# Kernel optimization log

Measured on AMD Instinct MI355X. Metric: run time of the kernel, lower is better.

The kernel has to match this reference:

```python
import jax, jax.numpy as jnp
import numpy as np

N_NODES = 50000
N_EDGES = 600000
N_GRAPHS = 500
HID = 128
N_LAYERS = 3
N_CLASSES = 10


def setup_inputs() -> dict:
    key = jax.random.key(0)
    ks = jax.random.split(key, 10)
    x = jax.random.normal(ks[0], (N_NODES, HID), dtype=jnp.float32)
    edge_attr = jax.random.normal(ks[1], (N_EDGES, 4), dtype=jnp.float32)
    edge_index = jax.random.randint(ks[2], (2, N_EDGES), 0, N_NODES, dtype=jnp.int32)
    batch = jnp.sort(jax.random.randint(ks[3], (N_NODES,), 0, N_GRAPHS, dtype=jnp.int32))
    s = 1.0 / np.sqrt(HID)
    Wl = jax.random.normal(ks[4], (N_LAYERS, HID, HID), dtype=jnp.float32) * s
    bl = jax.random.normal(ks[5], (N_LAYERS, HID), dtype=jnp.float32) * s
    Wr = jax.random.normal(ks[6], (N_LAYERS, HID, HID), dtype=jnp.float32) * s
    W1 = jax.random.normal(ks[7], (HID, HID), dtype=jnp.float32) * s
    b1 = jnp.zeros((HID,), dtype=jnp.float32)
    W2 = jax.random.normal(ks[8], (N_CLASSES, HID), dtype=jnp.float32) * s
    b2 = jnp.zeros((N_CLASSES,), dtype=jnp.float32)
    return {"x": x, "edge_attr": edge_attr, "edge_index": edge_index, "batch": batch,
            "Wl": Wl, "bl": bl, "Wr": Wr, "W1": W1, "b1": b1, "W2": W2, "b2": b2}


def _sage_conv(x, src, dst, Wl_i, bl_i, Wr_i):
    # mean aggregation of source-node features at target nodes (PyG SAGEConv)
    msg_sum = jax.ops.segment_sum(x[src], dst, num_segments=N_NODES)  # [N, H]
    cnt = jax.ops.segment_sum(jnp.ones((src.shape[0],), x.dtype), dst, num_segments=N_NODES)
    mean = msg_sum / jnp.maximum(cnt, 1.0)[:, None]
    return mean @ Wl_i.T + bl_i + x @ Wr_i.T


def reference(x, edge_attr, edge_index, batch, Wl, bl, Wr, W1, b1, W2, b2):
    # edge_attr is ignored by SAGEConv
    src, dst = edge_index[0], edge_index[1]
    for i in range(N_LAYERS):
        x = jax.nn.relu(_sage_conv(x, src, dst, Wl[i], bl[i], Wr[i]))
    # global_add_pool over graphs
    g = jax.ops.segment_sum(x, batch, num_segments=N_GRAPHS)  # [G, H]
    g = jax.nn.relu(g)
    # dropout p=0.5 is identity at inference
    h = jax.nn.relu(g @ W1.T + b1)
    logits = h @ W2.T + b2
    return jax.nn.log_softmax(logits, axis=1)
```

## Files before the change

### kernel.cpp

```cpp
#include <hip/hip_runtime.h>
#include <math.h>

#define HID 128
#define NCLS 10
#define MAXDEG 32
#define TROWS 64
#define MSP 136

typedef __attribute__((ext_vector_type(8))) short frag8;
typedef __attribute__((ext_vector_type(8))) unsigned short u16x8;
typedef __attribute__((ext_vector_type(2))) unsigned int u32x2;
typedef __attribute__((ext_vector_type(4))) float f32x4;

static __device__ __forceinline__ float relu_f(float v) { return v > 0.f ? v : 0.f; }

static __device__ __forceinline__ unsigned short f2bf(float f) {
    unsigned int u = __float_as_uint(f);
    u += 0x7fffu + ((u >> 16) & 1u);
    return (unsigned short)(u >> 16);
}
static __device__ __forceinline__ float bf2f(unsigned short u) {
    return __uint_as_float(((unsigned int)u) << 16);
}

static __device__ __forceinline__ unsigned int f2fp8x4(float a, float b, float c, float d) {
    int w = __builtin_amdgcn_cvt_pk_fp8_f32(a, b, 0, false);
    w = __builtin_amdgcn_cvt_pk_fp8_f32(c, d, w, true);
    return (unsigned int)w;
}
static __device__ __forceinline__ unsigned char f2fp8(float v) {
    return (unsigned char)(__builtin_amdgcn_cvt_pk_fp8_f32(v, v, 0, false) & 0xff);
}
static __device__ __forceinline__ void f8acc(unsigned int w0, unsigned int w1, float* acc) {
    auto p0 = __builtin_amdgcn_cvt_pk_f32_fp8((int)w0, false);
    auto p1 = __builtin_amdgcn_cvt_pk_f32_fp8((int)w0, true);
    auto p2 = __builtin_amdgcn_cvt_pk_f32_fp8((int)w1, false);
    auto p3 = __builtin_amdgcn_cvt_pk_f32_fp8((int)w1, true);
    acc[0] += p0[0]; acc[1] += p0[1]; acc[2] += p1[0]; acc[3] += p1[1];
    acc[4] += p2[0]; acc[5] += p2[1]; acc[6] += p3[0]; acc[7] += p3[1];
}

static __device__ __forceinline__ void conv4(const float* __restrict__ in,
                                             unsigned short* __restrict__ out, int i) {
    float4 v = *(const float4*)&in[i * 4];
    ushort4 o;
    o.x = f2bf(v.x); o.y = f2bf(v.y); o.z = f2bf(v.z); o.w = f2bf(v.w);
    *(ushort4*)&out[i * 4] = o;
}

__global__ __launch_bounds__(256) void prep_kernel(const float* __restrict__ x, unsigned short* __restrict__ xb,
                                                   unsigned int* __restrict__ xf8w, int nx4,
                                                   const float* __restrict__ Wl, unsigned short* __restrict__ wlb, int nwl4,
                                                   const float* __restrict__ Wr, unsigned short* __restrict__ wrb, int nwr4,
                                                   int* __restrict__ deg, int ndeg4,
                                                   uint4* __restrict__ colp, int ncol8, unsigned int zpat,
                                                   uint4* __restrict__ zp0, uint4* __restrict__ zp1,
                                                   uint4* __restrict__ zp2, int nz8,
                                                   uint4* __restrict__ zf0, uint4* __restrict__ zf1,
                                                   uint4* __restrict__ zf2) {
    int i = blockIdx.x * blockDim.x + threadIdx.x;
    if (i < nx4) {
        float4 v = *(const float4*)&x[i * 4];
        ushort4 o;
        o.x = f2bf(v.x); o.y = f2bf(v.y); o.z = f2bf(v.z); o.w = f2bf(v.w);
        *(ushort4*)&xb[i * 4] = o;
        xf8w[i] = f2fp8x4(v.x, v.y, v.z, v.w);
        return;
    }
    i -= nx4;
    if (i < nwl4) { conv4(Wl, wlb, i); return; }
    i -= nwl4;
    if (i < nwr4) { conv4(Wr, wrb, i); return; }
    i -= nwr4;
    if (i < ndeg4) { *(int4*)&deg[i * 4] = make_int4(0, 0, 0, 0); return; }
    i -= ndeg4;
    if (i < ncol8) { colp[i] = make_uint4(zpat, zpat, zpat, zpat); return; }
    i -= ncol8;
    if (i < nz8) { zp0[i] = make_uint4(0, 0, 0, 0); return; }
    i -= nz8;
    if (i < nz8) { zp1[i] = make_uint4(0, 0, 0, 0); return; }
    i -= nz8;
    if (i < nz8) { zp2[i] = make_uint4(0, 0, 0, 0); return; }
    i -= nz8;
    if (i < 8) { zf0[i] = make_uint4(0, 0, 0, 0); return; }
    i -= 8;
    if (i < 8) { zf1[i] = make_uint4(0, 0, 0, 0); return; }
    i -= 8;
    if (i < 8) zf2[i] = make_uint4(0, 0, 0, 0);
}

__global__ void fill_kernel(const int* __restrict__ src, const int* __restrict__ dst,
                            int* __restrict__ deg, unsigned short* __restrict__ col, int nE) {
    int e = blockIdx.x * blockDim.x + threadIdx.x;
    if (e < nE) {
        int d = dst[e];
        int p = atomicAdd(&deg[d], 1);
        if (p < MAXDEG) col[(long)d * MAXDEG + p] = (unsigned short)src[e];
    }
}

__global__ __launch_bounds__(256, 3) void sage_kernel(const unsigned short* __restrict__ Xb,
                                                      const unsigned char* __restrict__ Xf8,
                                                      const int* __restrict__ deg,
                                                      const unsigned short* __restrict__ col,
                                                      const unsigned short* __restrict__ Wlb,
                                                      const unsigned short* __restrict__ Wrb,
                                                      const float* __restrict__ bl,
                                                      unsigned short* __restrict__ Yb,
                                                      unsigned char* __restrict__ Yf8,
                                                      int wr8, int nN) {
    __shared__ unsigned short ms[TROWS * MSP];

    const int r0 = blockIdx.x * TROWS;

    {
        const int grp = threadIdx.x >> 4;
        const int l16 = threadIdx.x & 15;
        const int fo8 = l16 * 8;
        const long fo = (long)l16 * 8;

        for (int i = 0; i < 4; ++i) {
            const int nl = grp * 4 + i;
            const int n = r0 + nl;
            const int d = min(deg[n], MAXDEG);
            const unsigned short* cp = col + (long)n * MAXDEG;

            float acc[8] = {0, 0, 0, 0, 0, 0, 0, 0};

            if (d > 0) {
                u16x8 iv0 = *(const u16x8*)&cp[0];
                u16x8 iv1 = *(const u16x8*)&cp[8];
                u32x2 q[16];
#pragma unroll
                for (int k = 0; k < 8; ++k)
                    q[k] = *(const u32x2*)&Xf8[(long)iv0[k] * HID + fo8];
#pragma unroll
                for (int k = 0; k < 8; ++k)
                    q[8 + k] = *(const u32x2*)&Xf8[(long)iv1[k] * HID + fo8];
#pragma unroll
                for (int k = 0; k < 16; ++k) f8acc(q[k][0], q[k][1], acc);

                if (d > 16) {
                    u16x8 iv2 = *(const u16x8*)&cp[16];
                    u16x8 iv3 = *(const u16x8*)&cp[24];
#pragma unroll
                    for (int k = 0; k < 8; ++k)
                        q[k] = *(const u32x2*)&Xf8[(long)iv2[k] * HID + fo8];
#pragma unroll
                    for (int k = 0; k < 8; ++k)
                        q[8 + k] = *(const u32x2*)&Xf8[(long)iv3[k] * HID + fo8];
#pragma unroll
                    for (int k = 0; k < 16; ++k) f8acc(q[k][0], q[k][1], acc);
                }
            }

            const float inv = 1.f / fmaxf((float)d, 1.f);
            u16x8 o;
#pragma unroll
            for (int j = 0; j < 8; ++j) o[j] = f2bf(acc[j] * inv);
            *(u16x8*)&ms[nl * MSP + fo] = o;
        }
    }
    __syncthreads();

    const int lane = threadIdx.x & 63;
    const int wave = threadIdx.x >> 6;
    const int l15 = lane & 15;
    const int quad = lane >> 4;
    const int wr = wave & 1;
    const int wc = wave >> 1;

    f32x4 acc[2][4];
#pragma unroll
    for (int rt = 0; rt < 2; ++rt)
#pragma unroll
        for (int ct = 0; ct < 4; ++ct) acc[rt][ct] = (f32x4){0.f, 0.f, 0.f, 0.f};

#pragma unroll
    for (int ks = 0; ks < HID; ks += 32) {
        frag8 aM[2], aX[2];
#pragma unroll
        for (int rt = 0; rt < 2; ++rt) {
            const int lrow = wr * 32 + rt * 16 + l15;
            aM[rt] = *(const frag8*)&ms[lrow * MSP + ks + quad * 8];
            aX[rt] = *(const frag8*)&Xb[(long)(r0 + lrow) * HID + ks + quad * 8];
        }
#pragma unroll
        for (int ct = 0; ct < 4; ++ct) {
            const long nrow = wc * 64 + ct * 16 + l15;
            frag8 bL = *(const frag8*)&Wlb[nrow * HID + ks + quad * 8];
            frag8 bR = *(const frag8*)&Wrb[nrow * HID + ks + quad * 8];
#pragma unroll
            for (int rt = 0; rt < 2; ++rt) {
                acc[rt][ct] = __builtin_amdgcn_mfma_f32_16x16x32_bf16(aM[rt], bL, acc[rt][ct], 0, 0, 0);
                acc[rt][ct] = __builtin_amdgcn_mfma_f32_16x16x32_bf16(aX[rt], bR, acc[rt][ct], 0, 0, 0);
            }
        }
    }

#pragma unroll
    for (int ct = 0; ct < 4; ++ct) {
        const int gc = wc * 64 + ct * 16 + l15;
        const float bb = bl[gc];
#pragma unroll
        for (int rt = 0; rt < 2; ++rt) {
#pragma unroll
            for (int reg = 0; reg < 4; ++reg) {
                const int gm = r0 + wr * 32 + rt * 16 + quad * 4 + reg;
                if (gm < nN) {
                    const float v = relu_f(acc[rt][ct][reg] + bb);
                    Yb[(long)gm * HID + gc] = f2bf(v);
                    if (wr8) Yf8[(long)gm * HID + gc] = f2fp8(v);
                }
            }
        }
    }
}

__global__ __launch_bounds__(128) void poolmlp_kernel(const unsigned short* __restrict__ xb,
                                                      const int* __restrict__ batch, int nN,
                                                      const float* __restrict__ W1,
                                                      const float* __restrict__ b1,
                                                      const float* __restrict__ W2,
                                                      const float* __restrict__ b2,
                                                      float* __restrict__ out) {
    __shared__ float gs[HID];
    __shared__ float hs[HID];
    __shared__ float ls[NCLS];
    __shared__ float red[2];
    int gid = blockIdx.x;
    int j = threadIdx.x;

    int lo = 0, hi = nN;
    while (lo < hi) { int mid = (lo + hi) >> 1; if (batch[mid] < gid) lo = mid + 1; else hi = mid; }
    int s = lo;
    hi = nN;
    while (lo < hi) { int mid = (lo + hi) >> 1; if (batch[mid] < gid + 1) lo = mid + 1; else hi = mid; }
    int e = lo;

    float a0 = 0.f, a1 = 0.f, a2 = 0.f, a3 = 0.f;
    int n = s;
    for (; n + 4 <= e; n += 4) {
        a0 += bf2f(xb[(long)n * HID + j]);
        a1 += bf2f(xb[(long)(n + 1) * HID + j]);
        a2 += bf2f(xb[(long)(n + 2) * HID + j]);
        a3 += bf2f(xb[(long)(n + 3) * HID + j]);
    }
    for (; n < e; ++n) a0 += bf2f(xb[(long)n * HID + j]);
    gs[j] = relu_f((a0 + a1) + (a2 + a3));
    __syncthreads();

    float acc = b1[j];
#pragma unroll 8
    for (int k = 0; k < HID; ++k) acc += gs[k] * W1[j * HID + k];
    hs[j] = relu_f(acc);
    __syncthreads();
    if (j < NCLS) {
        float lg = b2[j];
#pragma unroll 8
        for (int k = 0; k < HID; ++k) lg += hs[k] * W2[j * HID + k];
        ls[j] = lg;
    }
    __syncthreads();
    if (j == 0) {
        float m = ls[0];
        for (int c = 1; c < NCLS; ++c) m = fmaxf(m, ls[c]);
        float sum = 0.f;
        for (int c = 0; c < NCLS; ++c) sum += expf(ls[c] - m);
        red[0] = m;
        red[1] = logf(sum);
    }
    __syncthreads();
    if (j < NCLS) out[gid * NCLS + j] = ls[j] - red[0] - red[1];
}


extern "C" void kernel_launch(void* const* d_in, const int* in_sizes, int n_in,
                              void* d_out, int out_size, void* d_ws, size_t ws_size,
                              hipStream_t stream) {
    const float* x_in  = (const float*)d_in[0];
    const int*   eidx  = (const int*)d_in[2];
    const int*   batch = (const int*)d_in[3];
    const float* Wl    = (const float*)d_in[4];
    const float* bl    = (const float*)d_in[5];
    const float* Wr    = (const float*)d_in[6];
    const float* W1    = (const float*)d_in[7];
    const float* b1    = (const float*)d_in[8];
    const float* W2    = (const float*)d_in[9];
    const float* b2    = (const float*)d_in[10];
    float* out = (float*)d_out;

    const int nN = in_sizes[0] / HID;
    const int nE = in_sizes[2] / 2;
    const int nG = out_size / NCLS;
    const int nWl = in_sizes[4];
    const int nWr = in_sizes[6];
    const int nNp = (nN + TROWS - 1) & ~(TROWS - 1);
    const int nTiles = nNp / TROWS;
    const int nRows = nNp + 8;

    const int* src = eidx;
    const int* dst = eidx + nE;

    char* p = (char*)d_ws;
    auto carve = [&](size_t bytes) {
        char* r = p;
        p += (bytes + 255) & ~(size_t)255;
        return r;
    };
    unsigned short* xb  = (unsigned short*)carve((size_t)nRows * HID * 2);
    unsigned short* yb0 = (unsigned short*)carve((size_t)nRows * HID * 2);
    unsigned short* yb1 = (unsigned short*)carve((size_t)nRows * HID * 2);
    unsigned char* xf8  = (unsigned char*)carve((size_t)(nNp + 1) * HID);
    unsigned char* yf80 = (unsigned char*)carve((size_t)(nNp + 1) * HID);
    unsigned char* yf81 = (unsigned char*)carve((size_t)(nNp + 1) * HID);
    unsigned short* wlb = (unsigned short*)carve((size_t)nWl * 2);
    unsigned short* wrb = (unsigned short*)carve((size_t)nWr * 2);
    int*   deg = (int*)carve((size_t)nNp * 4);
    unsigned short* col = (unsigned short*)carve((size_t)nNp * MAXDEG * 2);
    (void)ws_size; (void)n_in;

    const int nx4 = nN * HID / 4, nwl4 = nWl / 4, nwr4 = nWr / 4;
    const int ndeg4 = (nNp + 3) / 4;
    const int ncol8 = nNp * MAXDEG / 8;
    const int nzrows = nNp - nN;
    const int nz8 = (nzrows * HID) / 8;
    const unsigned int zpat = (unsigned int)nNp | ((unsigned int)nNp << 16);
    const int prep_total = nx4 + nwl4 + nwr4 + ndeg4 + ncol8 + 3 * nz8 + 24;
    prep_kernel<<<(prep_total + 255) / 256, 256, 0, stream>>>(
        x_in, xb, (unsigned int*)xf8, nx4, Wl, wlb, nwl4, Wr, wrb, nwr4, deg, ndeg4,
        (uint4*)col, ncol8, zpat,
        (uint4*)(xb + (size_t)nN * HID), (uint4*)(yb0 + (size_t)nN * HID),
        (uint4*)(yb1 + (size_t)nN * HID), nz8,
        (uint4*)(xf8 + (size_t)nNp * HID), (uint4*)(yf80 + (size_t)nNp * HID),
        (uint4*)(yf81 + (size_t)nNp * HID));

    fill_kernel<<<(nE + 255) / 256, 256, 0, stream>>>(src, dst, deg, col, nE);

    const unsigned short* xcur = xb;
    const unsigned char* fcur = xf8;
    unsigned short* bufs[2] = {yb0, yb1};
    unsigned char* fbufs[2] = {yf80, yf81};
    for (int l = 0; l < 3; ++l) {
        sage_kernel<<<nTiles, 256, 0, stream>>>(
            xcur, fcur, deg, col,
            wlb + (size_t)l * HID * HID, wrb + (size_t)l * HID * HID,
            bl + (size_t)l * HID, bufs[l & 1], fbufs[l & 1], (l < 2) ? 1 : 0, nN);
        xcur = bufs[l & 1];
        fcur = fbufs[l & 1];
    }

    poolmlp_kernel<<<nG, 128, 0, stream>>>(xcur, batch, nN, W1, b1, W2, b2, out);
}
```

Measured before the change: 266.6 us.

## Halve row tile to 32 and pin gather loads ahead of accumulation

The fused SAGE layer kernel now handles 32 rows per block instead of 64. Each thread gathers 2 nodes instead of 4, and each wave computes one 16-row MFMA tile instead of two. This doubles the block count and shrinks LDS and accumulator use, which should raise occupancy and latency hiding for the irregular neighbor gather. Scheduling barriers are added so all 16 gather loads are issued before the fp8 accumulation, at the cost of holding more registers and reading the weight fragments twice as often per row.

```diff
diff --git a/kernel.cpp b/kernel.cpp
--- a/kernel.cpp
+++ b/kernel.cpp
@@ -4,7 +4,7 @@
 #define HID 128
 #define NCLS 10
 #define MAXDEG 32
-#define TROWS 64
+#define TROWS 32
 #define MSP 136
 
 typedef __attribute__((ext_vector_type(8))) short frag8;
@@ -119,8 +119,8 @@
         const int fo8 = l16 * 8;
         const long fo = (long)l16 * 8;
 
-        for (int i = 0; i < 4; ++i) {
-            const int nl = grp * 4 + i;
+        for (int i = 0; i < 2; ++i) {
+            const int nl = grp * 2 + i;
             const int n = r0 + nl;
             const int d = min(deg[n], MAXDEG);
             const unsigned short* cp = col + (long)n * MAXDEG;
@@ -137,6 +137,7 @@
 #pragma unroll
                 for (int k = 0; k < 8; ++k)
                     q[8 + k] = *(const u32x2*)&Xf8[(long)iv1[k] * HID + fo8];
+                __builtin_amdgcn_sched_barrier(0);
 #pragma unroll
                 for (int k = 0; k < 16; ++k) f8acc(q[k][0], q[k][1], acc);
 
@@ -149,6 +150,7 @@
 #pragma unroll
                     for (int k = 0; k < 8; ++k)
                         q[8 + k] = *(const u32x2*)&Xf8[(long)iv3[k] * HID + fo8];
+                    __builtin_amdgcn_sched_barrier(0);
 #pragma unroll
                     for (int k = 0; k < 16; ++k) f8acc(q[k][0], q[k][1], acc);
                 }
@@ -170,31 +172,22 @@
     const int wr = wave & 1;
     const int wc = wave >> 1;
 
-    f32x4 acc[2][4];
-#pragma unroll
-    for (int rt = 0; rt < 2; ++rt)
-#pragma unroll
-        for (int ct = 0; ct < 4; ++ct) acc[rt][ct] = (f32x4){0.f, 0.f, 0.f, 0.f};
+    f32x4 acc[4];
+#pragma unroll
+    for (int ct = 0; ct < 4; ++ct) acc[ct] = (f32x4){0.f, 0.f, 0.f, 0.f};
 
 #pragma unroll
     for (int ks = 0; ks < HID; ks += 32) {
-        frag8 aM[2], aX[2];
-#pragma unroll
-        for (int rt = 0; rt < 2; ++rt) {
-            const int lrow = wr * 32 + rt * 16 + l15;
-            aM[rt] = *(const frag8*)&ms[lrow * MSP + ks + quad * 8];
-            aX[rt] = *(const frag8*)&Xb[(long)(r0 + lrow) * HID + ks + quad * 8];
-        }
+        const int lrow = wr * 16 + l15;
+        frag8 aM = *(const frag8*)&ms[lrow * MSP + ks + quad * 8];
+        frag8 aX = *(const frag8*)&Xb[(long)(r0 + lrow) * HID + ks + quad * 8];
 #pragma unroll
         for (int ct = 0; ct < 4; ++ct) {
             const long nrow = wc * 64 + ct * 16 + l15;
             frag8 bL = *(const frag8*)&Wlb[nrow * HID + ks + quad * 8];
             frag8 bR = *(const frag8*)&Wrb[nrow * HID + ks + quad * 8];
-#pragma unroll
-            for (int rt = 0; rt < 2; ++rt) {
-                acc[rt][ct] = __builtin_amdgcn_mfma_f32_16x16x32_bf16(aM[rt], bL, acc[rt][ct], 0, 0, 0);
-                acc[rt][ct] = __builtin_amdgcn_mfma_f32_16x16x32_bf16(aX[rt], bR, acc[rt][ct], 0, 0, 0);
-            }
+            acc[ct] = __builtin_amdgcn_mfma_f32_16x16x32_bf16(aM, bL, acc[ct], 0, 0, 0);
+            acc[ct] = __builtin_amdgcn_mfma_f32_16x16x32_bf16(aX, bR, acc[ct], 0, 0, 0);
         }
     }
 
@@ -203,15 +196,12 @@
         const int gc = wc * 64 + ct * 16 + l15;
         const float bb = bl[gc];
 #pragma unroll
-        for (int rt = 0; rt < 2; ++rt) {
-#pragma unroll
-            for (int reg = 0; reg < 4; ++reg) {
-                const int gm = r0 + wr * 32 + rt * 16 + quad * 4 + reg;
-                if (gm < nN) {
-                    const float v = relu_f(acc[rt][ct][reg] + bb);
-                    Yb[(long)gm * HID + gc] = f2bf(v);
-                    if (wr8) Yf8[(long)gm * HID + gc] = f2fp8(v);
-                }
+        for (int reg = 0; reg < 4; ++reg) {
+            const int gm = r0 + wr * 16 + quad * 4 + reg;
+            if (gm < nN) {
+                const float v = relu_f(acc[ct][reg] + bb);
+                Yb[(long)gm * HID + gc] = f2bf(v);
+                if (wr8) Yf8[(long)gm * HID + gc] = f2fp8(v);
             }
         }
     }
```

Result: slower. 290.4 us (+8.9%).

## Split fused SAGE layer into separate gather-aggregate and GEMM kernels

Applied to the files above, without the earlier changes.

The fused per-tile kernel is replaced by two kernels per layer. The first gathers and averages FP8 neighbour features into a bf16 mean buffer in global memory, one node per 16-lane group, with high occupancy and sched barriers to batch its loads. The second runs the dual bf16 MFMA GEMM with 128-row tiles, each wave covering all 128 output columns. This decouples the latency-bound gather from the compute phase so each can use its own occupancy. The cost is an extra global write and read of the mean tensor and two launches per layer instead of one.

```diff
diff --git a/kernel.cpp b/kernel.cpp
--- a/kernel.cpp
+++ b/kernel.cpp
@@ -4,8 +4,6 @@
 #define HID 128
 #define NCLS 10
 #define MAXDEG 32
-#define TROWS 64
-#define MSP 136
 
 typedef __attribute__((ext_vector_type(8))) short frag8;
 typedef __attribute__((ext_vector_type(8))) unsigned short u16x8;
@@ -99,95 +97,88 @@
     }
 }
 
-__global__ __launch_bounds__(256, 3) void sage_kernel(const unsigned short* __restrict__ Xb,
-                                                      const unsigned char* __restrict__ Xf8,
-                                                      const int* __restrict__ deg,
-                                                      const unsigned short* __restrict__ col,
-                                                      const unsigned short* __restrict__ Wlb,
-                                                      const unsigned short* __restrict__ Wrb,
-                                                      const float* __restrict__ bl,
-                                                      unsigned short* __restrict__ Yb,
-                                                      unsigned char* __restrict__ Yf8,
-                                                      int wr8, int nN) {
-    __shared__ unsigned short ms[TROWS * MSP];
-
-    const int r0 = blockIdx.x * TROWS;
-
-    {
-        const int grp = threadIdx.x >> 4;
-        const int l16 = threadIdx.x & 15;
-        const int fo8 = l16 * 8;
-        const long fo = (long)l16 * 8;
-
-        for (int i = 0; i < 4; ++i) {
-            const int nl = grp * 4 + i;
-            const int n = r0 + nl;
-            const int d = min(deg[n], MAXDEG);
-            const unsigned short* cp = col + (long)n * MAXDEG;
-
-            float acc[8] = {0, 0, 0, 0, 0, 0, 0, 0};
-
-            if (d > 0) {
-                u16x8 iv0 = *(const u16x8*)&cp[0];
-                u16x8 iv1 = *(const u16x8*)&cp[8];
-                u32x2 q[16];
-#pragma unroll
-                for (int k = 0; k < 8; ++k)
-                    q[k] = *(const u32x2*)&Xf8[(long)iv0[k] * HID + fo8];
-#pragma unroll
-                for (int k = 0; k < 8; ++k)
-                    q[8 + k] = *(const u32x2*)&Xf8[(long)iv1[k] * HID + fo8];
-#pragma unroll
-                for (int k = 0; k < 16; ++k) f8acc(q[k][0], q[k][1], acc);
-
-                if (d > 16) {
-                    u16x8 iv2 = *(const u16x8*)&cp[16];
-                    u16x8 iv3 = *(const u16x8*)&cp[24];
-#pragma unroll
-                    for (int k = 0; k < 8; ++k)
-                        q[k] = *(const u32x2*)&Xf8[(long)iv2[k] * HID + fo8];
-#pragma unroll
-                    for (int k = 0; k < 8; ++k)
-                        q[8 + k] = *(const u32x2*)&Xf8[(long)iv3[k] * HID + fo8];
-#pragma unroll
-                    for (int k = 0; k < 16; ++k) f8acc(q[k][0], q[k][1], acc);
-                }
-            }
-
-            const float inv = 1.f / fmaxf((float)d, 1.f);
-            u16x8 o;
-#pragma unroll
-            for (int j = 0; j < 8; ++j) o[j] = f2bf(acc[j] * inv);
-            *(u16x8*)&ms[nl * MSP + fo] = o;
+__global__ __launch_bounds__(256, 6) void agg_kernel(const unsigned char* __restrict__ Xf8,
+                                                     const int* __restrict__ deg,
+                                                     const unsigned short* __restrict__ col,
+                                                     unsigned short* __restrict__ meanb, int nNp) {
+    const int grp = threadIdx.x >> 4;
+    const int l16 = threadIdx.x & 15;
+    const int fo8 = l16 * 8;
+
+    const int n = blockIdx.x * 16 + grp;
+    const int d = min(deg[n], MAXDEG);
+    const unsigned short* cp = col + (long)n * MAXDEG;
+
+    float acc[8] = {0, 0, 0, 0, 0, 0, 0, 0};
+
+    if (d > 0) {
+        u16x8 iv0 = *(const u16x8*)&cp[0];
+        u16x8 iv1 = *(const u16x8*)&cp[8];
+        u32x2 q[16];
+#pragma unroll
+        for (int k = 0; k < 8; ++k)
+            q[k] = *(const u32x2*)&Xf8[(long)iv0[k] * HID + fo8];
+#pragma unroll
+        for (int k = 0; k < 8; ++k)
+            q[8 + k] = *(const u32x2*)&Xf8[(long)iv1[k] * HID + fo8];
+        __builtin_amdgcn_sched_barrier(0);
+#pragma unroll
+        for (int k = 0; k < 16; ++k) f8acc(q[k][0], q[k][1], acc);
+
+        if (d > 16) {
+            u16x8 iv2 = *(const u16x8*)&cp[16];
+            u16x8 iv3 = *(const u16x8*)&cp[24];
+#pragma unroll
+            for (int k = 0; k < 8; ++k)
+                q[k] = *(const u32x2*)&Xf8[(long)iv2[k] * HID + fo8];
+#pragma unroll
+            for (int k = 0; k < 8; ++k)
+                q[8 + k] = *(const u32x2*)&Xf8[(long)iv3[k] * HID + fo8];
+            __builtin_amdgcn_sched_barrier(0);
+#pragma unroll
+            for (int k = 0; k < 16; ++k) f8acc(q[k][0], q[k][1], acc);
         }
     }
-    __syncthreads();
-
-    const int lane = threadIdx.x & 63;
-    const int wave = threadIdx.x >> 6;
-    const int l15 = lane & 15;
-    const int quad = lane >> 4;
-    const int wr = wave & 1;
-    const int wc = wave >> 1;
-
-    f32x4 acc[2][4];
+
+    const float inv = 1.f / fmaxf((float)d, 1.f);
+    u16x8 o;
+#pragma unroll
+    for (int j = 0; j < 8; ++j) o[j] = f2bf(acc[j] * inv);
+    *(u16x8*)&meanb[(long)n * HID + fo8] = o;
+}
+
+__global__ __launch_bounds__(256) void gemm_kernel(const unsigned short* __restrict__ Ab,
+                                                   const unsigned short* __restrict__ Xb,
+                                                   const unsigned short* __restrict__ Wlb,
+                                                   const unsigned short* __restrict__ Wrb,
+                                                   const float* __restrict__ bl,
+                                                   unsigned short* __restrict__ Yb,
+                                                   unsigned char* __restrict__ Yf8,
+                                                   int wr8, int nN) {
+    int wave = threadIdx.x >> 6;
+    int lane = threadIdx.x & 63;
+    int l15 = lane & 15;
+    int quad = lane >> 4;
+    int r0 = blockIdx.x * 128 + wave * 32;
+
+    f32x4 acc[2][8];
 #pragma unroll
     for (int rt = 0; rt < 2; ++rt)
 #pragma unroll
-        for (int ct = 0; ct < 4; ++ct) acc[rt][ct] = (f32x4){0.f, 0.f, 0.f, 0.f};
+        for (int ct = 0; ct < 8; ++ct) acc[rt][ct] = (f32x4){0.f, 0.f, 0.f, 0.f};
 
 #pragma unroll
     for (int ks = 0; ks < HID; ks += 32) {
         frag8 aM[2], aX[2];
 #pragma unroll
         for (int rt = 0; rt < 2; ++rt) {
-            const int lrow = wr * 32 + rt * 16 + l15;
-            aM[rt] = *(const frag8*)&ms[lrow * MSP + ks + quad * 8];
-            aX[rt] = *(const frag8*)&Xb[(long)(r0 + lrow) * HID + ks + quad * 8];
+            long row = r0 + rt * 16 + l15;
+            aM[rt] = *(const frag8*)&Ab[row * HID + ks + quad * 8];
+            aX[rt] = *(const frag8*)&Xb[row * HID + ks + quad * 8];
         }
 #pragma unroll
-        for (int ct = 0; ct < 4; ++ct) {
-            const long nrow = wc * 64 + ct * 16 + l15;
+        for (int ct = 0; ct < 8; ++ct) {
+            long nrow = ct * 16 + l15;
             frag8 bL = *(const frag8*)&Wlb[nrow * HID + ks + quad * 8];
             frag8 bR = *(const frag8*)&Wrb[nrow * HID + ks + quad * 8];
 #pragma unroll
@@ -199,16 +190,16 @@
     }
 
 #pragma unroll
-    for (int ct = 0; ct < 4; ++ct) {
-        const int gc = wc * 64 + ct * 16 + l15;
-        const float bb = bl[gc];
+    for (int ct = 0; ct < 8; ++ct) {
+        float bb = bl[ct * 16 + l15];
 #pragma unroll
         for (int rt = 0; rt < 2; ++rt) {
 #pragma unroll
             for (int reg = 0; reg < 4; ++reg) {
-                const int gm = r0 + wr * 32 + rt * 16 + quad * 4 + reg;
+                int gm = r0 + rt * 16 + quad * 4 + reg;
                 if (gm < nN) {
-                    const float v = relu_f(acc[rt][ct][reg] + bb);
+                    float v = relu_f(acc[rt][ct][reg] + bb);
+                    int gc = ct * 16 + l15;
                     Yb[(long)gm * HID + gc] = f2bf(v);
                     if (wr8) Yf8[(long)gm * HID + gc] = f2fp8(v);
                 }
@@ -295,8 +286,7 @@
     const int nG = out_size / NCLS;
     const int nWl = in_sizes[4];
     const int nWr = in_sizes[6];
-    const int nNp = (nN + TROWS - 1) & ~(TROWS - 1);
-    const int nTiles = nNp / TROWS;
+    const int nNp = (nN + 127) & ~127;
     const int nRows = nNp + 8;
 
     const int* src = eidx;
@@ -308,9 +298,10 @@
         p += (bytes + 255) & ~(size_t)255;
         return r;
     };
-    unsigned short* xb  = (unsigned short*)carve((size_t)nRows * HID * 2);
-    unsigned short* yb0 = (unsigned short*)carve((size_t)nRows * HID * 2);
-    unsigned short* yb1 = (unsigned short*)carve((size_t)nRows * HID * 2);
+    unsigned short* xb    = (unsigned short*)carve((size_t)nRows * HID * 2);
+    unsigned short* yb0   = (unsigned short*)carve((size_t)nRows * HID * 2);
+    unsigned short* yb1   = (unsigned short*)carve((size_t)nRows * HID * 2);
+    unsigned short* meanb = (unsigned short*)carve((size_t)nRows * HID * 2);
     unsigned char* xf8  = (unsigned char*)carve((size_t)(nNp + 1) * HID);
     unsigned char* yf80 = (unsigned char*)carve((size_t)(nNp + 1) * HID);
     unsigned char* yf81 = (unsigned char*)carve((size_t)(nNp + 1) * HID);
@@ -342,8 +333,9 @@
     unsigned short* bufs[2] = {yb0, yb1};
     unsigned char* fbufs[2] = {yf80, yf81};
     for (int l = 0; l < 3; ++l) {
-        sage_kernel<<<nTiles, 256, 0, stream>>>(
-            xcur, fcur, deg, col,
+        agg_kernel<<<nNp / 16, 256, 0, stream>>>(fcur, deg, col, meanb, nNp);
+        gemm_kernel<<<nNp / 128, 256, 0, stream>>>(
+            meanb, xcur,
             wlb + (size_t)l * HID * HID, wrb + (size_t)l * HID * HID,
             bl + (size_t)l * HID, bufs[l & 1], fbufs[l & 1], (l < 2) ? 1 : 0, nN);
         xcur = bufs[l & 1];
```

New measurement: 282.9 us. 6.1% more time.
